# Kernel tuning notes

Measured on AMD Instinct MI355X. Metric: run time of the kernel, lower is better.

## Reference

```python
import jax, jax.numpy as jnp
import numpy as np

B, P, D = 32, 64, 34
L = 1048576  # 1024x1024 flattened locations


def setup_inputs() -> dict:
    key = jax.random.key(0)
    k1, k2, k3, k4 = jax.random.split(key, 4)
    preds = jax.random.normal(k1, (B, L), dtype=jnp.float32)
    vals = jax.random.normal(k2, (B, P, D), dtype=jnp.float32)
    idx = jax.random.randint(k3, (B, P, D), 0, L).astype(jnp.float32)
    # valid flag > 0 with prob ~0.7; guarantee each image has at least one valid entry
    flags = jax.random.uniform(k4, (B, P, D), dtype=jnp.float32) - 0.3
    flags = flags.at[:, 0, 0].set(1.0)
    gts = jnp.stack([vals, idx, flags], axis=-1)  # [B, P, D, 3]
    return {"preds": preds, "gts": gts}


def reference(preds, gts):
    # gts[..., 0] = target value, gts[..., 1] = flat index into preds, gts[..., 2] = valid flag
    vals = gts[..., 0]                      # [B, P, D]
    idx = gts[..., 1].astype(jnp.int32)     # [B, P, D]
    valid = gts[..., 2] > 0                 # [B, P, D]
    b = preds.shape[0]
    gathered = jnp.take_along_axis(preds, idx.reshape(b, -1), axis=1).reshape(idx.shape)
    per = jnp.where(valid, jnp.abs(gathered - vals), jnp.zeros((), preds.dtype))
    # num_people = persons with at least one valid dim (others are skipped in the loop)
    num_people = jnp.sum(jnp.any(valid, axis=-1), axis=-1).astype(preds.dtype)  # [B]
    return jnp.sum(per, axis=(1, 2)) / num_people  # [B]
```

## Files before the change

kernel.cpp:

```cpp
#include <hip/hip_runtime.h>


#define B_ 32
#define P_ 64
#define D_ 34
#define L_ 1048576

__global__ __launch_bounds__(256) void reg_l1_kernel(
    const float* __restrict__ preds,
    const float* __restrict__ gts,
    float* __restrict__ out) {
  const int b   = blockIdx.x;
  const int tid = threadIdx.x;
  const int p   = tid >> 2;
  const int sub = tid & 3;

  const float* pred_b = preds + (size_t)b * L_;
  const float* gt_p   = gts + (((size_t)b * P_ + p) * D_) * 3;

  float sum = 0.0f;
  int any = 0;
  for (int d = sub; d < D_; d += 4) {
    const float v    = gt_p[d * 3 + 0];
    const float fidx = gt_p[d * 3 + 1];
    const float flag = gt_p[d * 3 + 2];
    if (flag > 0.0f) {
      const int idx = (int)fidx;
      const float g = pred_b[idx];
      sum += fabsf(g - v);
      any = 1;
    }
  }

  sum += __shfl_xor(sum, 1);
  sum += __shfl_xor(sum, 2);
  any |= __shfl_xor(any, 1);
  any |= __shfl_xor(any, 2);

  float psum = (sub == 0) ? sum        : 0.0f;
  float pcnt = (sub == 0) ? (float)any : 0.0f;

  for (int off = 4; off < 64; off <<= 1) {
    psum += __shfl_xor(psum, off);
    pcnt += __shfl_xor(pcnt, off);
  }

  __shared__ float s_sum[4];
  __shared__ float s_cnt[4];
  const int wave = tid >> 6;
  const int lane = tid & 63;
  if (lane == 0) {
    s_sum[wave] = psum;
    s_cnt[wave] = pcnt;
  }
  __syncthreads();
  if (tid == 0) {
    const float ts = s_sum[0] + s_sum[1] + s_sum[2] + s_sum[3];
    const float tc = s_cnt[0] + s_cnt[1] + s_cnt[2] + s_cnt[3];
    out[b] = ts / tc;
  }
}

extern "C" void kernel_launch(void* const* d_in, const int* in_sizes, int n_in,
                              void* d_out, int out_size, void* d_ws, size_t ws_size,
                              hipStream_t stream) {
  const float* preds = (const float*)d_in[0];
  const float* gts   = (const float*)d_in[1];
  float* out = (float*)d_out;
  reg_l1_kernel<<<B_, 256, 0, stream>>>(preds, gts, out);
}
```

Baseline: 172.0 us.

## Split per-image work across 16 blocks per image and add a final reduction kernel

```diff
diff --git a/kernel.cpp b/kernel.cpp
--- a/kernel.cpp
+++ b/kernel.cpp
@@ -5,60 +5,67 @@
 #define P_ 64
 #define D_ 34
 #define L_ 1048576
+#define GPB 4
+#define BLK_PER_IMG (P_ / GPB)
 
-__global__ __launch_bounds__(256) void reg_l1_kernel(
+__global__ __launch_bounds__(256) void reg_l1_main(
     const float* __restrict__ preds,
     const float* __restrict__ gts,
-    float* __restrict__ out) {
-  const int b   = blockIdx.x;
-  const int tid = threadIdx.x;
-  const int p   = tid >> 2;
-  const int sub = tid & 3;
+    float* __restrict__ ws) {
+  const int g    = blockIdx.x;
+  const int b    = blockIdx.y;
+  const int wave = threadIdx.x >> 6;
+  const int lane = threadIdx.x & 63;
+  const int p    = g * GPB + wave;
 
-  const float* pred_b = preds + (size_t)b * L_;
-  const float* gt_p   = gts + (((size_t)b * P_ + p) * D_) * 3;
-
-  float sum = 0.0f;
-  int any = 0;
-  for (int d = sub; d < D_; d += 4) {
-    const float v    = gt_p[d * 3 + 0];
-    const float fidx = gt_p[d * 3 + 1];
-    const float flag = gt_p[d * 3 + 2];
+  float contrib = 0.0f;
+  int valid = 0;
+  if (lane < D_) {
+    const float* gt = gts + (((size_t)b * P_ + p) * D_ + lane) * 3;
+    const float v    = gt[0];
+    const float fidx = gt[1];
+    const float flag = gt[2];
     if (flag > 0.0f) {
       const int idx = (int)fidx;
-      const float g = pred_b[idx];
-      sum += fabsf(g - v);
-      any = 1;
+      contrib = fabsf(preds[(size_t)b * L_ + idx] - v);
+      valid = 1;
     }
   }
 
-  sum += __shfl_xor(sum, 1);
-  sum += __shfl_xor(sum, 2);
-  any |= __shfl_xor(any, 1);
-  any |= __shfl_xor(any, 2);
+  for (int off = 1; off < 64; off <<= 1) contrib += __shfl_xor(contrib, off);
+  const unsigned long long bal = __ballot(valid);
+  const float pcnt = (bal != 0ull) ? 1.0f : 0.0f;
 
-  float psum = (sub == 0) ? sum        : 0.0f;
-  float pcnt = (sub == 0) ? (float)any : 0.0f;
-
-  for (int off = 4; off < 64; off <<= 1) {
-    psum += __shfl_xor(psum, off);
-    pcnt += __shfl_xor(pcnt, off);
-  }
-
-  __shared__ float s_sum[4];
-  __shared__ float s_cnt[4];
-  const int wave = tid >> 6;
-  const int lane = tid & 63;
+  __shared__ float s_sum[GPB];
+  __shared__ float s_cnt[GPB];
   if (lane == 0) {
-    s_sum[wave] = psum;
+    s_sum[wave] = contrib;
     s_cnt[wave] = pcnt;
   }
   __syncthreads();
-  if (tid == 0) {
+  if (threadIdx.x == 0) {
     const float ts = s_sum[0] + s_sum[1] + s_sum[2] + s_sum[3];
     const float tc = s_cnt[0] + s_cnt[1] + s_cnt[2] + s_cnt[3];
-    out[b] = ts / tc;
+    ws[b * BLK_PER_IMG + g] = ts;
+    ws[B_ * BLK_PER_IMG + b * BLK_PER_IMG + g] = tc;
   }
+}
+
+__global__ __launch_bounds__(64) void reg_l1_final(
+    const float* __restrict__ ws,
+    float* __restrict__ out) {
+  const int b    = blockIdx.x;
+  const int lane = threadIdx.x;
+  float s = 0.0f, c = 0.0f;
+  if (lane < BLK_PER_IMG) {
+    s = ws[b * BLK_PER_IMG + lane];
+    c = ws[B_ * BLK_PER_IMG + b * BLK_PER_IMG + lane];
+  }
+  for (int off = 1; off < BLK_PER_IMG; off <<= 1) {
+    s += __shfl_xor(s, off);
+    c += __shfl_xor(c, off);
+  }
+  if (lane == 0) out[b] = s / c;
 }
 
 extern "C" void kernel_launch(void* const* d_in, const int* in_sizes, int n_in,
@@ -67,5 +74,9 @@
   const float* preds = (const float*)d_in[0];
   const float* gts   = (const float*)d_in[1];
   float* out = (float*)d_out;
-  reg_l1_kernel<<<B_, 256, 0, stream>>>(preds, gts, out);
+  float* ws  = (float*)d_ws;
+
+  dim3 grid(BLK_PER_IMG, B_);
+  reg_l1_main<<<grid, 256, 0, stream>>>(preds, gts, ws);
+  reg_l1_final<<<B_, 64, 0, stream>>>(ws, out);
 }
```

Result: faster. 164.1 us, median of 2 (-4.6%).
